# Performance work log

Measured on AMD Instinct MI355X. Metric: run time of the kernel, lower is better.

The kernel has to match this reference:

```python
import jax, jax.numpy as jnp
import numpy as np

WINDOW = 14

def _make_rel_index(ws):
    coords = np.stack(np.meshgrid(np.arange(ws), np.arange(ws), indexing='ij'))  # [2,ws,ws]
    flat = coords.reshape(2, -1)
    rel = flat[:, :, None] - flat[:, None, :]            # [2,N,N]
    rel = rel.transpose(1, 2, 0).copy()
    rel[:, :, 0] += ws - 1
    rel[:, :, 1] += ws - 1
    rel[:, :, 0] *= 2 * ws - 1
    return rel.sum(-1).astype(np.int32)                  # [N,N]

def setup_inputs() -> dict:
    key = jax.random.key(0)
    ks = jax.random.split(key, 7)
    B, N, C, H = 256, WINDOW * WINDOW, 768, 12
    s = 0.02
    return {
        'x': jax.random.normal(ks[0], (B, N, C), jnp.float32),
        'qkv_w': jax.random.normal(ks[1], (3 * C, C), jnp.float32) * s,
        'q_bias': jnp.zeros((C,), jnp.float32),
        'v_bias': jnp.zeros((C,), jnp.float32),
        'rpb_table': jax.random.normal(ks[2], ((2 * WINDOW - 1) ** 2, H), jnp.float32) * s,
        'proj_w': jax.random.normal(ks[3], (C, C), jnp.float32) * s,
        'proj_b': jnp.zeros((C,), jnp.float32),
        'rel_index': jnp.asarray(_make_rel_index(WINDOW)),
        'num_heads': H,
    }

def reference(x, qkv_w, q_bias, v_bias, rpb_table, proj_w, proj_b, rel_index, num_heads):
    B, N, C = x.shape
    H = num_heads
    hd = C // H
    scale = hd ** -0.5
    qkv_bias = jnp.concatenate([q_bias, jnp.zeros_like(v_bias), v_bias])
    qkv = x @ qkv_w.T + qkv_bias                          # [B,N,3C]
    qkv = qkv.reshape(B, N, 3, H, hd).transpose(2, 0, 3, 1, 4)  # [3,B,H,N,hd]
    q, k, v = qkv[0] * scale, qkv[1], qkv[2]
    attn = jnp.einsum('bhnd,bhmd->bhnm', q, k)            # [B,H,N,N]
    rpb = rpb_table[rel_index.reshape(-1)].reshape(N, N, H).transpose(2, 0, 1)  # [H,N,N]
    attn = jax.nn.softmax(attn + rpb, axis=-1)
    out = jnp.einsum('bhnm,bhmd->bhnd', attn, v)          # [B,H,N,hd]
    out = out.transpose(0, 2, 1, 3).reshape(B, N, C)
    return out @ proj_w.T + proj_b
```

## Files before the change

kernel.cpp:

```cpp
#include <hip/hip_runtime.h>
#include <hip/hip_fp16.h>

typedef _Float16 f16;
typedef __attribute__((ext_vector_type(8))) _Float16 f16x8;
typedef __attribute__((ext_vector_type(4))) float f32x4;

#define MFMA16 __builtin_amdgcn_mfma_f32_16x16x32_f16
#define BAR() __builtin_amdgcn_s_barrier()
#define VMCNT(n) asm volatile("s_waitcnt vmcnt(" #n ")" ::: "memory")
#define LGKM(n) asm volatile("s_waitcnt lgkmcnt(" #n ")" ::: "memory")
#define SCHEDB() __builtin_amdgcn_sched_barrier(0)

__device__ __forceinline__ void gload16(const f16* g, char* l) {
  __builtin_amdgcn_global_load_lds(
      (const __attribute__((address_space(1))) void*)g,
      (__attribute__((address_space(3))) void*)l, 16, 0, 0);
}

__global__ __launch_bounds__(256) void cvt_k(const float* __restrict__ in,
                                             f16* __restrict__ out, int n8) {
  int i = blockIdx.x * 256 + threadIdx.x;
  const int stride = gridDim.x * 256;
  for (; i < n8; i += stride) {
    const f32x4* p = (const f32x4*)(in + (size_t)i * 8);
    f32x4 a = __builtin_nontemporal_load(p);
    f32x4 b = __builtin_nontemporal_load(p + 1);
    f16x8 h;
    h[0] = (f16)a[0]; h[1] = (f16)a[1]; h[2] = (f16)a[2]; h[3] = (f16)a[3];
    h[4] = (f16)b[0]; h[5] = (f16)b[1]; h[6] = (f16)b[2]; h[7] = (f16)b[3];
    *(f16x8*)(out + (size_t)i * 8) = h;
  }
}

__global__ __launch_bounds__(256) void rpb_build_k(const float* __restrict__ tab,
                                                   const int* __restrict__ rel,
                                                   f16* __restrict__ out) {
  int i = blockIdx.x * 256 + threadIdx.x;
  if (i >= 196 * 196) return;
  int idx = __builtin_nontemporal_load(rel + i);
#pragma unroll
  for (int h = 0; h < 12; ++h)
    out[h * (196 * 196) + i] = (f16)tab[idx * 12 + h];
}

template <int MODE>
__global__ __launch_bounds__(512) void gemm_k(
    const f16* __restrict__ A, const f16* __restrict__ W,
    const float* __restrict__ bias_a, const float* __restrict__ bias_b,
    f16* __restrict__ q_out, f16* __restrict__ k_out, f16* __restrict__ vT_out,
    float* __restrict__ f_out) {
  constexpr int NTIL = (MODE == 0) ? 9 : 3;
  constexpr int NWG = 196 * NTIL;
  constexpr int QX = NWG / 8, RX = NWG % 8;
  constexpr int KT = 12;

  extern __shared__ char lds[];

  const int tid = threadIdx.x;
  const int lane = tid & 63, wid = tid >> 6;
  const int xcd = blockIdx.x & 7, bix = blockIdx.x >> 3;
  const int lbid =
      (xcd < RX ? xcd * (QX + 1) : RX * (QX + 1) + (xcd - RX) * QX) + bix;
  const int brow = lbid / NTIL, bcol = lbid % NTIL;
  const int wr = wid >> 2, wc = wid & 3;
  const int l15 = lane & 15, g4 = lane >> 4;

  const int sr = wid * 8 + (lane >> 3);
  const int scw = ((lane & 7) ^ (lane >> 3)) * 8;
  const f16* pAt = A + (size_t)(brow * 256 + sr) * 768 + scw;
  const f16* pBt = W + (size_t)(bcol * 256 + sr) * 768 + scw;
  char* ldsW = lds + wid * 1024;

  auto stA = [&](int kt, int hf, int buf) {
#pragma unroll
    for (int i = 0; i < 2; ++i)
      gload16(pAt + (size_t)(hf * 128 + i * 64) * 768 + kt * 64,
              ldsW + buf * 65536 + hf * 16384 + i * 8192);
  };
  auto stB = [&](int kt, int hf, int buf) {
#pragma unroll
    for (int i = 0; i < 2; ++i)
      gload16(pBt + (size_t)(hf * 128 + i * 64) * 768 + kt * 64,
              ldsW + buf * 65536 + 32768 + hf * 16384 + i * 8192);
  };

  f16x8 af[2][4][2], bf[2][2][2];
  const int aswz = l15 & 7;
  const char* ldsAl = lds + (size_t)(wr * 128 + l15) * 128;
  const char* ldsBl = lds + 32768 + (size_t)(wc * 64 + l15) * 128;

  auto rdA = [&](int q, int buf) {
#pragma unroll
    for (int mf = 0; mf < 4; ++mf)
#pragma unroll
      for (int ks = 0; ks < 2; ++ks)
        af[q][mf][ks] = *(const f16x8*)(ldsAl + buf * 65536 +
                                        (q * 64 + mf * 16) * 128 +
                                        ((ks * 4 + g4) ^ aswz) * 16);
  };
  auto rdB = [&](int r, int buf) {
#pragma unroll
    for (int nf = 0; nf < 2; ++nf)
#pragma unroll
      for (int ks = 0; ks < 2; ++ks)
        bf[r][nf][ks] = *(const f16x8*)(ldsBl + buf * 65536 +
                                        (r * 32 + nf * 16) * 128 +
                                        ((ks * 4 + g4) ^ aswz) * 16);
  };

  const f32x4 zero4 = {0.f, 0.f, 0.f, 0.f};
  f32x4 acc[8][4];
#pragma unroll
  for (int i = 0; i < 8; ++i)
#pragma unroll
    for (int j = 0; j < 4; ++j) acc[i][j] = zero4;

  auto mm = [&](int q, int r) {
#pragma unroll
    for (int ks = 0; ks < 2; ++ks)
#pragma unroll
      for (int mf = 0; mf < 4; ++mf)
#pragma unroll
        for (int nf = 0; nf < 2; ++nf)
          acc[q * 4 + mf][r * 2 + nf] =
              MFMA16(af[q][mf][ks], bf[r][nf][ks], acc[q * 4 + mf][r * 2 + nf],
                     0, 0, 0);
  };

  stA(0, 0, 0); stA(0, 1, 0); stB(0, 0, 0); stB(0, 1, 0);
  VMCNT(0);
  BAR();

  for (int t = 0; t < KT; ++t) {
    const int cur = t & 1, nxt = cur ^ 1;
    if (t + 1 < KT) {
      stA(t + 1, 0, nxt); stA(t + 1, 1, nxt);
      stB(t + 1, 0, nxt); stB(t + 1, 1, nxt);
      VMCNT(8);
    } else {
      VMCNT(0);
    }
    BAR();
    rdA(0, cur); rdB(0, cur);
    SCHEDB();
    rdA(1, cur); rdB(1, cur);
    LGKM(12);
    SCHEDB();
    __builtin_amdgcn_s_setprio(1); mm(0, 0); mm(0, 1); __builtin_amdgcn_s_setprio(0);
    LGKM(0);
    SCHEDB();
    __builtin_amdgcn_s_setprio(1); mm(1, 0); mm(1, 1); __builtin_amdgcn_s_setprio(0);
    BAR();
  }

#pragma unroll
  for (int mf = 0; mf < 8; ++mf) {
    const int rowo = wr * 128 + (mf >> 2) * 64 + (mf & 3) * 16 + g4 * 4;
#pragma unroll
    for (int rr = 0; rr < 4; ++rr) {
      const int grow = brow * 256 + rowo + rr;
      if constexpr (MODE == 0) {
        const int bI = grow / 196;
        const int nI = grow - bI * 196;
#pragma unroll
        for (int nf = 0; nf < 4; ++nf) {
          const int col = bcol * 256 + wc * 64 + (nf >> 1) * 32 + (nf & 1) * 16 + l15;
          const int s = bcol / 3;
          const int rem = col - s * 768;
          const int hh = rem >> 6, dd = rem & 63;
          float v = acc[mf][nf][rr];
          if (s == 0) {
            v = (v + bias_a[rem]) * 0.125f;
            q_out[(((size_t)bI * 12 + hh) * 196 + nI) * 64 + dd] = (f16)v;
          } else if (s == 1) {
            k_out[(((size_t)bI * 12 + hh) * 196 + nI) * 64 + dd] = (f16)v;
          } else {
            v += bias_b[rem];
            vT_out[(((size_t)bI * 12 + hh) * 64 + dd) * 224 + nI] = (f16)v;
          }
        }
      } else {
        float* orow = f_out + (size_t)grow * 768;
#pragma unroll
        for (int nf = 0; nf < 4; ++nf) {
          const int col = bcol * 256 + wc * 64 + (nf >> 1) * 32 + (nf & 1) * 16 + l15;
          orow[col] = acc[mf][nf][rr] + bias_a[col];
        }
      }
    }
  }
}

__global__ __launch_bounds__(256) void attn_k(const f16* __restrict__ qg,
                                              const f16* __restrict__ kg,
                                              const f16* __restrict__ vTg,
                                              const f16* __restrict__ rpb,
                                              f16* __restrict__ og) {
  extern __shared__ char smem[];
  f16x8* Vlds = (f16x8*)smem;
  f16x8* Plds = (f16x8*)(smem + 32768);

  const int tid = threadIdx.x;
  const int bh = blockIdx.x;
  const int b = bh / 12, h = bh - b * 12;
  const int lane = tid & 63, wid = tid >> 6;
  const int l15 = lane & 15, g4 = lane >> 4;

  f16x8 z8;
#pragma unroll
  for (int j = 0; j < 8; ++j) z8[j] = (f16)0.f;

  const f16* vgb = vTg + (size_t)bh * (64 * 224);
  for (int c = tid; c < 64 * 32; c += 256) {
    int d = c >> 5, mc = c & 31;
    f16x8 v;
    if (mc < 24) {
      v = *(const f16x8*)(vgb + d * 224 + mc * 8);
    } else if (mc == 24) {
      v = *(const f16x8*)(vgb + d * 224 + mc * 8);
#pragma unroll
      for (int j = 4; j < 8; ++j) v[j] = (f16)0.f;
    } else {
      v = z8;
    }
    Vlds[d * 32 + (mc ^ (d & 7))] = v;
  }
  f16x8* Pw = Plds + wid * (16 * 32);
  if (g4 < 2) {
    int n = l15;
    Pw[n * 32 + ((26 + g4) ^ (n & 7))] = z8;
  }
  __syncthreads();

  const f16* qgb = qg + (size_t)bh * (196 * 64);
  const f16* kgb = kg + (size_t)bh * (196 * 64);
  const f16* rpbh = rpb + (size_t)h * (196 * 196);

  for (int rt = wid; rt < 13; rt += 4) {
    const int n0 = rt * 16;
    f16x8 qf0 = *(const f16x8*)(qgb + (n0 + l15) * 64 + g4 * 8);
    f16x8 qf1 = *(const f16x8*)(qgb + (n0 + l15) * 64 + 32 + g4 * 8);

    float rv[13][4];
#pragma unroll
    for (int mt = 0; mt < 13; ++mt) {
      const int m = mt * 16 + l15;
      const int mcl = (m < 196) ? m : 195;
#pragma unroll
      for (int r = 0; r < 4; ++r) {
        const int n = n0 + g4 * 4 + r;
        const int ncl = (n < 196) ? n : 195;
        rv[mt][r] = (float)rpbh[ncl * 196 + mcl];
      }
    }

    const f32x4 zero4 = {0.f, 0.f, 0.f, 0.f};
    f32x4 s[13];
#pragma unroll
    for (int mt = 0; mt < 13; ++mt) {
      const int m = mt * 16 + l15;
      f16x8 k0 = *(const f16x8*)(kgb + m * 64 + g4 * 8);
      f16x8 k1 = *(const f16x8*)(kgb + m * 64 + 32 + g4 * 8);
      s[mt] = MFMA16(qf0, k0, zero4, 0, 0, 0);
      s[mt] = MFMA16(qf1, k1, s[mt], 0, 0, 0);
    }

    float mx[4] = {-3e38f, -3e38f, -3e38f, -3e38f};
#pragma unroll
    for (int mt = 0; mt < 13; ++mt) {
      const int m = mt * 16 + l15;
#pragma unroll
      for (int r = 0; r < 4; ++r) {
        const int n = n0 + g4 * 4 + r;
        float v = (m < 196 && n < 196) ? s[mt][r] + rv[mt][r] : -1e30f;
        s[mt][r] = v;
        mx[r] = fmaxf(mx[r], v);
      }
    }
#pragma unroll
    for (int r = 0; r < 4; ++r) {
      mx[r] = fmaxf(mx[r], __shfl_xor(mx[r], 1));
      mx[r] = fmaxf(mx[r], __shfl_xor(mx[r], 2));
      mx[r] = fmaxf(mx[r], __shfl_xor(mx[r], 4));
      mx[r] = fmaxf(mx[r], __shfl_xor(mx[r], 8));
    }
    float sm[4] = {0.f, 0.f, 0.f, 0.f};
#pragma unroll
    for (int mt = 0; mt < 13; ++mt)
#pragma unroll
      for (int r = 0; r < 4; ++r) {
        float p = __expf(s[mt][r] - mx[r]);
        s[mt][r] = p;
        sm[r] += p;
      }
#pragma unroll
    for (int r = 0; r < 4; ++r) {
      sm[r] += __shfl_xor(sm[r], 1);
      sm[r] += __shfl_xor(sm[r], 2);
      sm[r] += __shfl_xor(sm[r], 4);
      sm[r] += __shfl_xor(sm[r], 8);
    }
    float rinv[4];
#pragma unroll
    for (int r = 0; r < 4; ++r) rinv[r] = 1.f / sm[r];

#pragma unroll
    for (int mt = 0; mt < 13; ++mt) {
      const int m = mt * 16 + l15;
#pragma unroll
      for (int r = 0; r < 4; ++r) {
        const int n = g4 * 4 + r;
        f16* dst = (f16*)Pw + n * 256 + (((m >> 3) ^ (n & 7)) << 3) + (m & 7);
        *dst = (f16)s[mt][r];
      }
    }

    f32x4 o[4];
#pragma unroll
    for (int dt = 0; dt < 4; ++dt) o[dt] = zero4;
#pragma unroll
    for (int ks = 0; ks < 7; ++ks) {
      f16x8 pa = Pw[l15 * 32 + ((ks * 4 + g4) ^ (l15 & 7))];
#pragma unroll
      for (int dt = 0; dt < 4; ++dt) {
        const int d = dt * 16 + l15;
        f16x8 vf = Vlds[d * 32 + ((ks * 4 + g4) ^ (d & 7))];
        o[dt] = MFMA16(pa, vf, o[dt], 0, 0, 0);
      }
    }

#pragma unroll
    for (int r = 0; r < 4; ++r) {
      const int n = n0 + g4 * 4 + r;
      if (n < 196) {
        f16* orow = og + ((size_t)b * 196 + n) * 768 + h * 64;
#pragma unroll
        for (int dt = 0; dt < 4; ++dt)
          orow[dt * 16 + l15] = (f16)(o[dt][r] * rinv[r]);
      }
    }
  }
}

extern "C" void kernel_launch(void* const* d_in, const int* in_sizes, int n_in,
                              void* d_out, int out_size, void* d_ws, size_t ws_size,
                              hipStream_t stream) {
  const float* x = (const float*)d_in[0];
  const float* qkv_w = (const float*)d_in[1];
  const float* q_bias = (const float*)d_in[2];
  const float* v_bias = (const float*)d_in[3];
  const float* rpb_tab = (const float*)d_in[4];
  const float* proj_w = (const float*)d_in[5];
  const float* proj_b = (const float*)d_in[6];
  const int* rel = (const int*)d_in[7];
  float* out = (float*)d_out;

  const size_t SZ_Q = 77070336;
  const size_t SZ_K = 77070336;
  const size_t SZ_VT = 88080384;
  const size_t SZ_AO = 77070336;
  const size_t SZ_RP = 921984;
  const size_t SZ_WQ = 3538944;
  const size_t SZ_WP = 1179648;
  if (ws_size < SZ_Q + SZ_K + SZ_VT + SZ_AO + SZ_RP + SZ_WQ + SZ_WP) return;

  char* w = (char*)d_ws;
  f16* q_ = (f16*)w;
  f16* k_ = (f16*)(w + SZ_Q);
  f16* vT_ = (f16*)(w + SZ_Q + SZ_K);
  f16* ao_ = (f16*)(w + SZ_Q + SZ_K + SZ_VT);
  f16* rp_ = (f16*)(w + SZ_Q + SZ_K + SZ_VT + SZ_AO);
  f16* whq_ = (f16*)(w + SZ_Q + SZ_K + SZ_VT + SZ_AO + SZ_RP);
  f16* whp_ = (f16*)(w + SZ_Q + SZ_K + SZ_VT + SZ_AO + SZ_RP + SZ_WQ);
  f16* xh_ = ao_;

  (void)hipFuncSetAttribute((const void*)attn_k,
                            hipFuncAttributeMaxDynamicSharedMemorySize, 65536);
  (void)hipFuncSetAttribute((const void*)gemm_k<0>,
                            hipFuncAttributeMaxDynamicSharedMemorySize, 131072);
  (void)hipFuncSetAttribute((const void*)gemm_k<1>,
                            hipFuncAttributeMaxDynamicSharedMemorySize, 131072);

  cvt_k<<<2048, 256, 0, stream>>>(x, xh_, 50176 * 768 / 8);
  cvt_k<<<864, 256, 0, stream>>>(qkv_w, whq_, 2304 * 768 / 8);
  cvt_k<<<288, 256, 0, stream>>>(proj_w, whp_, 768 * 768 / 8);
  rpb_build_k<<<(196 * 196 + 255) / 256, 256, 0, stream>>>(rpb_tab, rel, rp_);

  gemm_k<0><<<1764, 512, 131072, stream>>>(xh_, whq_, q_bias, v_bias,
                                           q_, k_, vT_, nullptr);
  attn_k<<<3072, 256, 65536, stream>>>(q_, k_, vT_, rp_, ao_);
  gemm_k<1><<<588, 512, 131072, stream>>>(ao_, whp_, proj_b, nullptr,
                                          nullptr, nullptr, nullptr, out);
}
```

Baseline: 803.2 us.

## Triple-buffer A and double-buffer B tiles to drop trailing GEMM barrier

Restructures the GEMM mainloop's LDS pipeline: A tiles rotate through three buffers and B tiles through two, with prefetch issued right after the barrier. This removes the second barrier per k-iteration and keeps loads two steps ahead for A. LDS use grows from 128KB to 160KB per block, and correctness now depends on the buffer rotation avoiding write-after-read hazards on B with only one barrier per iteration.

```diff
diff --git a/kernel.cpp b/kernel.cpp
--- a/kernel.cpp
+++ b/kernel.cpp
@@ -71,40 +71,40 @@
   const f16* pBt = W + (size_t)(bcol * 256 + sr) * 768 + scw;
   char* ldsW = lds + wid * 1024;
 
-  auto stA = [&](int kt, int hf, int buf) {
-#pragma unroll
-    for (int i = 0; i < 2; ++i)
-      gload16(pAt + (size_t)(hf * 128 + i * 64) * 768 + kt * 64,
-              ldsW + buf * 65536 + hf * 16384 + i * 8192);
-  };
-  auto stB = [&](int kt, int hf, int buf) {
-#pragma unroll
-    for (int i = 0; i < 2; ++i)
-      gload16(pBt + (size_t)(hf * 128 + i * 64) * 768 + kt * 64,
-              ldsW + buf * 65536 + 32768 + hf * 16384 + i * 8192);
+  auto stA = [&](int kt) {
+    char* base = ldsW + (kt % 3) * 32768;
+#pragma unroll
+    for (int i = 0; i < 4; ++i)
+      gload16(pAt + (size_t)(i * 64) * 768 + kt * 64, base + i * 8192);
+  };
+  auto stB = [&](int kt) {
+    char* base = ldsW + 98304 + (kt & 1) * 32768;
+#pragma unroll
+    for (int i = 0; i < 4; ++i)
+      gload16(pBt + (size_t)(i * 64) * 768 + kt * 64, base + i * 8192);
   };
 
   f16x8 af[2][4][2], bf[2][2][2];
   const int aswz = l15 & 7;
   const char* ldsAl = lds + (size_t)(wr * 128 + l15) * 128;
-  const char* ldsBl = lds + 32768 + (size_t)(wc * 64 + l15) * 128;
-
-  auto rdA = [&](int q, int buf) {
+  const char* ldsBl = lds + 98304 + (size_t)(wc * 64 + l15) * 128;
+
+  auto rdA = [&](int q, int t) {
+    const char* b = ldsAl + (t % 3) * 32768;
 #pragma unroll
     for (int mf = 0; mf < 4; ++mf)
 #pragma unroll
       for (int ks = 0; ks < 2; ++ks)
-        af[q][mf][ks] = *(const f16x8*)(ldsAl + buf * 65536 +
-                                        (q * 64 + mf * 16) * 128 +
+        af[q][mf][ks] = *(const f16x8*)(b + (q * 64 + mf * 16) * 128 +
                                         ((ks * 4 + g4) ^ aswz) * 16);
   };
-  auto rdB = [&](int r, int buf) {
+  auto rdB = [&](int r, int t) {
+    const char* b = ldsBl + (t & 1) * 32768;
 #pragma unroll
     for (int nf = 0; nf < 2; ++nf)
 #pragma unroll
       for (int ks = 0; ks < 2; ++ks)
-        bf[r][nf][ks] = *(const f16x8*)(ldsBl + buf * 65536 +
-                                        (r * 32 + nf * 16) * 128 +
+        bf[r][nf][ks] = *(const f16x8*)(b + (r * 32 + nf * 16) * 128 +
                                         ((ks * 4 + g4) ^ aswz) * 16);
   };
 
@@ -127,30 +127,22 @@
                      0, 0, 0);
   };
 
-  stA(0, 0, 0); stA(0, 1, 0); stB(0, 0, 0); stB(0, 1, 0);
-  VMCNT(0);
-  BAR();
+  stA(0); stB(0); stA(1);
 
   for (int t = 0; t < KT; ++t) {
-    const int cur = t & 1, nxt = cur ^ 1;
-    if (t + 1 < KT) {
-      stA(t + 1, 0, nxt); stA(t + 1, 1, nxt);
-      stB(t + 1, 0, nxt); stB(t + 1, 1, nxt);
-      VMCNT(8);
-    } else {
-      VMCNT(0);
-    }
+    if (t == KT - 1) { VMCNT(0); } else { VMCNT(4); }
     BAR();
-    rdA(0, cur); rdB(0, cur);
+    if (t + 1 < KT) stB(t + 1);
+    if (t + 2 < KT) stA(t + 2);
+    rdA(0, t); rdB(0, t);
     SCHEDB();
-    rdA(1, cur); rdB(1, cur);
+    rdA(1, t); rdB(1, t);
     LGKM(12);
     SCHEDB();
     __builtin_amdgcn_s_setprio(1); mm(0, 0); mm(0, 1); __builtin_amdgcn_s_setprio(0);
     LGKM(0);
     SCHEDB();
     __builtin_amdgcn_s_setprio(1); mm(1, 0); mm(1, 1); __builtin_amdgcn_s_setprio(0);
-    BAR();
   }
 
 #pragma unroll
@@ -377,18 +369,18 @@
   (void)hipFuncSetAttribute((const void*)attn_k,
                             hipFuncAttributeMaxDynamicSharedMemorySize, 65536);
   (void)hipFuncSetAttribute((const void*)gemm_k<0>,
-                            hipFuncAttributeMaxDynamicSharedMemorySize, 131072);
+                            hipFuncAttributeMaxDynamicSharedMemorySize, 163840);
   (void)hipFuncSetAttribute((const void*)gemm_k<1>,
-                            hipFuncAttributeMaxDynamicSharedMemorySize, 131072);
+                            hipFuncAttributeMaxDynamicSharedMemorySize, 163840);
 
   cvt_k<<<2048, 256, 0, stream>>>(x, xh_, 50176 * 768 / 8);
   cvt_k<<<864, 256, 0, stream>>>(qkv_w, whq_, 2304 * 768 / 8);
   cvt_k<<<288, 256, 0, stream>>>(proj_w, whp_, 768 * 768 / 8);
   rpb_build_k<<<(196 * 196 + 255) / 256, 256, 0, stream>>>(rpb_tab, rel, rp_);
 
-  gemm_k<0><<<1764, 512, 131072, stream>>>(xh_, whq_, q_bias, v_bias,
+  gemm_k<0><<<1764, 512, 163840, stream>>>(xh_, whq_, q_bias, v_bias,
                                            q_, k_, vT_, nullptr);
   attn_k<<<3072, 256, 65536, stream>>>(q_, k_, vT_, rp_, ao_);
-  gemm_k<1><<<588, 512, 131072, stream>>>(ao_, whp_, proj_b, nullptr,
+  gemm_k<1><<<588, 512, 163840, stream>>>(ao_, whp_, proj_b, nullptr,
                                           nullptr, nullptr, nullptr, out);
 }
```

Result: faster. 767.4 us (-4.5%).
